# Kernel tuning notes

Measured on AMD Instinct MI355X. Metric: run time of the kernel, lower is better.

## Reference

```python
import jax, jax.numpy as jnp
import numpy as np
from jax import lax

BS, T, NN, F_IN = 4, 32, 128, 64
HID, HEADS, NC, LD, RH = 64, 4, 32, 64, 256
E = 2048
NEG_SLOPE = 0.2


def setup_inputs() -> dict:
    key = jax.random.key(0)
    ks = jax.random.split(key, 20)
    f32 = jnp.float32
    def n(k, shape, s=0.05):
        return jax.random.normal(k, shape, f32) * s
    G4 = 4 * RH
    return {
        "x": jax.random.normal(ks[0], (BS, T, NN, F_IN), f32),
        "edge_index": jax.random.randint(ks[1], (2, E), 0, NN),
        "W1": n(ks[2], (F_IN, HEADS * HID)),
        "as1": n(ks[3], (HEADS, HID)), "ad1": n(ks[4], (HEADS, HID)),
        "b1": jnp.zeros((HEADS * HID,), f32),
        "W2": n(ks[5], (HEADS * HID, HEADS * HID)),
        "as2": n(ks[6], (HEADS, HID)), "ad2": n(ks[7], (HEADS, HID)),
        "b2": jnp.zeros((HEADS * HID,), f32),
        "W3": n(ks[8], (HEADS * HID, HID)),
        "as3": n(ks[9], (1, HID)), "ad3": n(ks[10], (1, HID)),
        "b3": jnp.zeros((HID,), f32),
        "Wih_f": n(ks[11], (G4, HID)), "Whh_f": n(ks[12], (G4, RH)),
        "bih_f": jnp.zeros((G4,), f32), "bhh_f": jnp.zeros((G4,), f32),
        "Wih_b": n(ks[13], (G4, HID)), "Whh_b": n(ks[14], (G4, RH)),
        "bih_b": jnp.zeros((G4,), f32), "bhh_b": jnp.zeros((G4,), f32),
        "Wmu": n(ks[15], (NC * LD, 2 * RH)), "bmu": jnp.zeros((NC * LD,), f32),
        "Wlv": n(ks[16], (NC * LD, 2 * RH)), "blv": jnp.zeros((NC * LD,), f32),
        "Wpi": n(ks[17], (NC, 2 * RH)), "bpi": jnp.zeros((NC,), f32),
    }


def _lstm_dir(seq, Wih, Whh, bih, bhh, rh):
    # seq: [T, B, D]; torch gate order i, f, g, o
    B = seq.shape[1]
    h0 = jnp.zeros((B, rh), seq.dtype)
    c0 = jnp.zeros((B, rh), seq.dtype)
    def step(carry, xt):
        h, c = carry
        g = xt @ Wih.T + h @ Whh.T + bih + bhh
        i, f, gg, o = jnp.split(g, 4, axis=-1)
        c = jax.nn.sigmoid(f) * c + jax.nn.sigmoid(i) * jnp.tanh(gg)
        h = jax.nn.sigmoid(o) * jnp.tanh(c)
        return (h, c), None
    (hT, _), _ = lax.scan(step, (h0, c0), seq)
    return hT


def reference(x, edge_index, W1, as1, ad1, b1, W2, as2, ad2, b2,
              W3, as3, ad3, b3,
              Wih_f, Whh_f, bih_f, bhh_f, Wih_b, Whh_b, bih_b, bhh_b,
              Wmu, bmu, Wlv, blv, Wpi, bpi):
    bs, T_, nn_, fin = x.shape
    G = bs * T_
    N = G * nn_
    xt = x.reshape(N, fin)
    # batch the per-graph edge list with node offsets, then add self loops (PyG default)
    off = jnp.arange(G, dtype=edge_index.dtype) * nn_
    src = (edge_index[0][None, :] + off[:, None]).reshape(-1)
    dst = (edge_index[1][None, :] + off[:, None]).reshape(-1)
    loop = jnp.arange(N, dtype=edge_index.dtype)
    src = jnp.concatenate([src, loop])
    dst = jnp.concatenate([dst, loop])

    def gat(h_in, W, a_s, a_d, b, heads):
        C = W.shape[1] // heads
        h = (h_in @ W).reshape(N, heads, C)
        a_src = jnp.sum(h * a_s, axis=-1)  # [N, H]
        a_dst = jnp.sum(h * a_d, axis=-1)
        e = jax.nn.leaky_relu(a_src[src] + a_dst[dst], NEG_SLOPE)  # [Etot, H]
        m = jax.ops.segment_max(e, dst, num_segments=N)
        m = jnp.where(jnp.isfinite(m), m, 0.0)
        ex = jnp.exp(e - m[dst])
        den = jax.ops.segment_sum(ex, dst, num_segments=N)
        alpha = ex / (den[dst] + 1e-16)
        out = jax.ops.segment_sum(alpha[:, :, None] * h[src], dst, num_segments=N)
        return out.reshape(N, heads * C) + b

    h = jax.nn.relu(gat(xt, W1, as1, ad1, b1, HEADS))
    h = jax.nn.relu(gat(h, W2, as2, ad2, b2, HEADS))
    h = jax.nn.relu(gat(h, W3, as3, ad3, b3, 1))

    batch_idx = jnp.repeat(jnp.arange(G), nn_)
    graph_embs = jax.ops.segment_sum(h, batch_idx, num_segments=G).reshape(bs, T_, -1)
    seq = jnp.transpose(graph_embs, (1, 0, 2))  # [T, B, D]
    h_f = _lstm_dir(seq, Wih_f, Whh_f, bih_f, bhh_f, RH)
    h_b = _lstm_dir(seq[::-1], Wih_b, Whh_b, bih_b, bhh_b, RH)
    feat = jnp.concatenate([h_f, h_b], axis=-1)  # [B, 2*RH]
    mu = (feat @ Wmu.T + bmu).reshape(bs, NC, LD)
    logvar = (feat @ Wlv.T + blv).reshape(bs, NC, LD)
    pi_logits = feat @ Wpi.T + bpi
    return (mu, logvar, pi_logits)
```

## Files before the change

### kernel.cpp

```cpp
#include <hip/hip_runtime.h>
#include <hip/hip_bf16.h>
#include <cstdint>

#define NLOC 128
#define NGRAPH 128
#define NNODE 16384
#define EBASE 2048

typedef _Float16 half2v __attribute__((ext_vector_type(2)));
typedef _Float16 f16x8 __attribute__((ext_vector_type(8)));
typedef float f32x4 __attribute__((ext_vector_type(4)));

__device__ __forceinline__ float sigf(float x) { return 1.f / (1.f + __expf(-x)); }
__device__ __forceinline__ float tanhfast(float x) {
    float e = __expf(2.f * x);
    return 1.f - 2.f / (e + 1.f);
}
__device__ __forceinline__ uint32_t packh2(float a, float b) {
    half2v v;
    v.x = (_Float16)a; v.y = (_Float16)b;
    return __builtin_bit_cast(uint32_t, v);
}
__device__ __forceinline__ float dot2(uint32_t w, uint32_t h, float acc) {
#if __has_builtin(__builtin_amdgcn_fdot2)
    return __builtin_amdgcn_fdot2(__builtin_bit_cast(half2v, w),
                                  __builtin_bit_cast(half2v, h), acc, false);
#else
    half2v wv = __builtin_bit_cast(half2v, w);
    half2v hv = __builtin_bit_cast(half2v, h);
    return acc + (float)wv.x * (float)hv.x + (float)wv.y * (float)hv.y;
#endif
}

__global__ __launch_bounds__(256) void prep_kernel(const int* __restrict__ ei,
                                                   float* __restrict__ Adj,
                                                   const float* __restrict__ W1,
                                                   const float* __restrict__ W2,
                                                   const float* __restrict__ W3,
                                                   _Float16* __restrict__ W1t,
                                                   _Float16* __restrict__ W2t,
                                                   _Float16* __restrict__ W3t,
                                                   const float* __restrict__ Whh_f,
                                                   const float* __restrict__ Whh_b,
                                                   uint32_t* __restrict__ wreg,
                                                   uint32_t* __restrict__ wtail) {
    int b = blockIdx.x, tid = threadIdx.x;
    if (b < 128) {
        __shared__ int rowA[NLOC];
        int v = b;
        if (tid < NLOC) rowA[tid] = 0;
        __syncthreads();
        const int* srcs = ei;
        const int* dsts = ei + EBASE;
        int e0 = tid * 8;
#pragma unroll
        for (int k = 0; k < 8; ++k)
            if (dsts[e0 + k] == v) atomicAdd(&rowA[srcs[e0 + k]], 1);
        __syncthreads();
        if (tid < NLOC) Adj[v * NLOC + tid] = (float)rowA[tid] + (tid == v ? 1.f : 0.f);
    } else if (b < 144) {
        int i = (b - 128) * 1024 + tid * 4;
        int n = i >> 6, k = i & 63;
#pragma unroll
        for (int j = 0; j < 4; ++j) W1t[n * 64 + k + j] = (_Float16)W1[(size_t)(k + j) * 256 + n];
    } else if (b < 208) {
        int i = (b - 144) * 1024 + tid * 4;
        int n = i >> 8, k = i & 255;
#pragma unroll
        for (int j = 0; j < 4; ++j) W2t[n * 256 + k + j] = (_Float16)W2[(size_t)(k + j) * 256 + n];
    } else if (b < 224) {
        int i = (b - 208) * 1024 + tid * 4;
        int n = i >> 8, k = i & 255;
#pragma unroll
        for (int j = 0; j < 4; ++j) W3t[n * 256 + k + j] = (_Float16)W3[(size_t)(k + j) * 64 + n];
    } else {
        int gid = (b - 224) * 256 + tid;
        int dir = gid >> 10, row = gid & 1023;
        const float* src = (dir ? Whh_b : Whh_f) + (size_t)row * 256;
        uint4* wr4 = (uint4*)wreg;
#pragma unroll
        for (int i = 0; i < 24; ++i) {
            uint4 v;
            v.x = packh2(src[i * 8 + 0], src[i * 8 + 1]);
            v.y = packh2(src[i * 8 + 2], src[i * 8 + 3]);
            v.z = packh2(src[i * 8 + 4], src[i * 8 + 5]);
            v.w = packh2(src[i * 8 + 6], src[i * 8 + 7]);
            wr4[(size_t)(dir * 24 + i) * 1024 + row] = v;
        }
        uint4* wt4 = (uint4*)wtail;
#pragma unroll
        for (int ku = 0; ku < 8; ++ku) {
            const float* s8 = src + 192 + ku * 8;
            uint4 v;
            v.x = packh2(s8[0], s8[1]);
            v.y = packh2(s8[2], s8[3]);
            v.z = packh2(s8[4], s8[5]);
            v.w = packh2(s8[6], s8[7]);
            wt4[(size_t)(dir * 8 + ku) * 1024 + row] = v;
        }
    }
}

template <int K, int N, bool POOLX>
__global__ __launch_bounds__(512) void fl_kernel(const float* __restrict__ A,
                                                 const _Float16* __restrict__ Wg,
                                                 const float* __restrict__ a_s,
                                                 const float* __restrict__ a_d,
                                                 const float* __restrict__ Adj,
                                                 const float* __restrict__ bias,
                                                 const float* __restrict__ Wih_f, const float* __restrict__ bif, const float* __restrict__ bhf,
                                                 const float* __restrict__ Wih_b, const float* __restrict__ bib, const float* __restrict__ bhb,
                                                 float* __restrict__ outG) {
    constexpr int H = N / 64;
    constexpr int NT = N / 64;
    constexpr int LDA = K + 4;
    constexpr int LDB = 68;
    constexpr int LDH = 136;
    constexpr int ASB = 128 * LDA * 2;
    constexpr int HTB = N * LDH * 2;
    constexpr int R1 = (ASB > HTB) ? ASB : HTB;
    constexpr int R2 = 128 * LDH * 2;
    __shared__ __align__(16) char raw[R1 + R2];
    _Float16* As = (_Float16*)raw;
    _Float16* Ht = (_Float16*)raw;
    _Float16* Bs = (_Float16*)(raw + R1);
    _Float16* Wt = (_Float16*)(raw + R1);
    __shared__ float as_l[128 * H];
    __shared__ float ad_l[128 * H];
    __shared__ float den_l[128];
    __shared__ float as_part[4][128];
    __shared__ float ad_part[4][128];
    __shared__ float psum[8][64];
    __shared__ float emb[64];

    int g = blockIdx.x, tid = threadIdx.x;
    int lane = tid & 63, w = tid >> 6;
    int wm = w >> 2, wn = w & 3;
    int col = lane & 15, kg = lane >> 4;
    size_t base = (size_t)g * 128;

    float asc[NT], adc[NT];
#pragma unroll
    for (int nt = 0; nt < NT; ++nt) {
        int f = (wn * NT + nt) * 16 + col;
        asc[nt] = a_s[f];
        adc[nt] = a_d[f];
    }
    {
        const float* src = A + base * K;
        for (int i = tid; i < 128 * K / 2; i += 512) {
            int m = (2 * i) / K, k = (2 * i) % K;
            float2 v = *(const float2*)(src + (size_t)m * K + k);
            *(uint32_t*)&As[m * LDA + k] = packh2(v.x, v.y);
        }
    }
    f32x4 acc[4][NT];
#pragma unroll
    for (int mt = 0; mt < 4; ++mt)
#pragma unroll
        for (int nt = 0; nt < NT; ++nt) acc[mt][nt] = (f32x4){0.f, 0.f, 0.f, 0.f};
#pragma unroll 1
    for (int kc = 0; kc < K / 64; ++kc) {
        __syncthreads();
        for (int j = tid; j < N * 8; j += 512) {
            int n = j >> 3, ko = (j & 7) * 8;
            *(uint4*)&Bs[n * LDB + ko] = *(const uint4*)&Wg[(size_t)n * K + kc * 64 + ko];
        }
        __syncthreads();
        uint4 bf[NT][2];
#pragma unroll
        for (int nt = 0; nt < NT; ++nt) {
            int nb = (wn * NT + nt) * 16 + col;
            bf[nt][0] = *(const uint4*)&Bs[nb * LDB + kg * 8];
            bf[nt][1] = *(const uint4*)&Bs[nb * LDB + 32 + kg * 8];
        }
#pragma unroll
        for (int mt = 0; mt < 4; ++mt) {
            int mrow = wm * 64 + mt * 16 + col;
            uint4 a0 = *(const uint4*)&As[mrow * LDA + kc * 64 + kg * 8];
            uint4 a1 = *(const uint4*)&As[mrow * LDA + kc * 64 + 32 + kg * 8];
#pragma unroll
            for (int nt = 0; nt < NT; ++nt) {
                acc[mt][nt] = __builtin_amdgcn_mfma_f32_16x16x32_f16(
                    __builtin_bit_cast(f16x8, a0), __builtin_bit_cast(f16x8, bf[nt][0]),
                    acc[mt][nt], 0, 0, 0);
                acc[mt][nt] = __builtin_amdgcn_mfma_f32_16x16x32_f16(
                    __builtin_bit_cast(f16x8, a1), __builtin_bit_cast(f16x8, bf[nt][1]),
                    acc[mt][nt], 0, 0, 0);
            }
        }
    }
    __syncthreads();
#pragma unroll
    for (int mt = 0; mt < 4; ++mt) {
        int mb = wm * 64 + mt * 16;
        float pas[4] = {0.f, 0.f, 0.f, 0.f}, pdd[4] = {0.f, 0.f, 0.f, 0.f};
#pragma unroll
        for (int nt = 0; nt < NT; ++nt) {
#pragma unroll
            for (int r = 0; r < 4; ++r) {
                float hv = acc[mt][nt][r];
                pas[r] += hv * asc[nt];
                pdd[r] += hv * adc[nt];
            }
            int f = (wn * NT + nt) * 16 + col;
            *(uint32_t*)&Ht[f * LDH + mb + kg * 4] = packh2(acc[mt][nt][0], acc[mt][nt][1]);
            *(uint32_t*)&Ht[f * LDH + mb + kg * 4 + 2] = packh2(acc[mt][nt][2], acc[mt][nt][3]);
        }
#pragma unroll
        for (int off = 1; off < 16; off <<= 1)
#pragma unroll
            for (int r = 0; r < 4; ++r) {
                pas[r] += __shfl_xor(pas[r], off, 64);
                pdd[r] += __shfl_xor(pdd[r], off, 64);
            }
        if (col == 0) {
#pragma unroll
            for (int r = 0; r < 4; ++r) {
                int m = mb + kg * 4 + r;
                if constexpr (N == 256) {
                    as_l[m * 4 + wn] = pas[r];
                    ad_l[m * 4 + wn] = pdd[r];
                } else {
                    as_part[wn][m] = pas[r];
                    ad_part[wn][m] = pdd[r];
                }
            }
        }
    }
    __syncthreads();
    if constexpr (N == 64) {
        if (tid < 128) {
            as_l[tid] = as_part[0][tid] + as_part[1][tid] + as_part[2][tid] + as_part[3][tid];
            ad_l[tid] = ad_part[0][tid] + ad_part[1][tid] + ad_part[2][tid] + ad_part[3][tid];
        }
        __syncthreads();
    }
    for (int h = 0; h < H; ++h) {
        {
            int v = tid >> 2, ub = (tid & 3) * 32;
            float advv = ad_l[v * H + h];
            const float* arow = Adj + (size_t)v * 128 + ub;
            float dsum = 0.f;
#pragma unroll
            for (int j = 0; j < 16; ++j) {
                float a0 = arow[2 * j], a1 = arow[2 * j + 1];
                float e0 = as_l[(ub + 2 * j) * H + h] + advv;
                float e1 = as_l[(ub + 2 * j + 1) * H + h] + advv;
                e0 = (e0 > 0.f) ? e0 : 0.2f * e0;
                e1 = (e1 > 0.f) ? e1 : 0.2f * e1;
                float w0 = a0 * __expf(e0);
                float w1 = a1 * __expf(e1);
                dsum += w0 + w1;
                *(uint32_t*)&Wt[v * LDH + ub + 2 * j] = packh2(w0, w1);
            }
            dsum += __shfl_xor(dsum, 1, 64);
            dsum += __shfl_xor(dsum, 2, 64);
            if ((tid & 3) == 0) den_l[v] = dsum;
        }
        __syncthreads();
        {
            int vt = w;
            f16x8 af[4];
#pragma unroll
            for (int kt = 0; kt < 4; ++kt) {
                uint4 au = *(const uint4*)&Wt[(vt * 16 + col) * LDH + kt * 32 + kg * 8];
                af[kt] = __builtin_bit_cast(f16x8, au);
            }
            float dn[4];
#pragma unroll
            for (int r = 0; r < 4; ++r) dn[r] = den_l[vt * 16 + kg * 4 + r] + 1e-16f;
#pragma unroll
            for (int ft = 0; ft < 4; ++ft) {
                int f = h * 64 + ft * 16 + col;
                f32x4 oacc = {0.f, 0.f, 0.f, 0.f};
#pragma unroll
                for (int kt = 0; kt < 4; ++kt) {
                    uint4 bu = *(const uint4*)&Ht[f * LDH + kt * 32 + kg * 8];
                    oacc = __builtin_amdgcn_mfma_f32_16x16x32_f16(
                        af[kt], __builtin_bit_cast(f16x8, bu), oacc, 0, 0, 0);
                }
                float bv = bias[f];
                if constexpr (!POOLX) {
#pragma unroll
                    for (int r = 0; r < 4; ++r) {
                        int v = vt * 16 + kg * 4 + r;
                        float o = oacc[r] / dn[r] + bv;
                        outG[(size_t)(base + v) * N + f] = fmaxf(o, 0.f);
                    }
                } else {
                    float ps = 0.f;
#pragma unroll
                    for (int r = 0; r < 4; ++r) ps += fmaxf(oacc[r] / dn[r] + bv, 0.f);
                    ps += __shfl_xor(ps, 16, 64);
                    ps += __shfl_xor(ps, 32, 64);
                    if (kg == 0) psum[w][f] = ps;
                }
            }
        }
        __syncthreads();
    }
    if constexpr (POOLX) {
        if (tid < 64) {
            float s = 0.f;
#pragma unroll
            for (int q = 0; q < 8; ++q) s += psum[q][tid];
            emb[tid] = s;
        }
        __syncthreads();
        int rrow = (g & 31) * 4 + (g >> 5);
        for (int dir = 0; dir < 2; ++dir) {
            const float* W = dir ? Wih_b : Wih_f;
            const float* bi = dir ? bib : bif;
            const float* bh = dir ? bhb : bhf;
            for (int o = tid; o < 1024; o += 512) {
                const float* wr = W + (size_t)o * 64;
                float s = bi[o] + bh[o];
#pragma unroll
                for (int k = 0; k < 64; k += 4) {
                    float4 wv = *(const float4*)(wr + k);
                    s += emb[k] * wv.x + emb[k + 1] * wv.y + emb[k + 2] * wv.z + emb[k + 3] * wv.w;
                }
                outG[dir * 131072 + rrow * 1024 + o] = s;
            }
        }
    }
}

__global__ __launch_bounds__(1024, 1) void lstm_kernel(const float* __restrict__ xp,
                                                       const uint32_t* __restrict__ wreg,
                                                       const uint32_t* __restrict__ wtail,
                                                       float* __restrict__ hT) {
    int blk = blockIdx.x;
    int dir = blk >> 2, batch = blk & 3;
    int t = threadIdx.x;
    uint32_t wa[96];
    {
        const uint4* ra = (const uint4*)wreg + (size_t)dir * 24 * 1024;
#pragma unroll
        for (int i = 0; i < 24; ++i) {
            uint4 v = ra[i * 1024 + t];
            wa[i * 4 + 0] = v.x; wa[i * 4 + 1] = v.y; wa[i * 4 + 2] = v.z; wa[i * 4 + 3] = v.w;
        }
    }
    __shared__ __align__(16) uint4 wlds[8 * 1024];
    __shared__ __align__(16) uint32_t h_pk[128];
    __shared__ float gv[1024];
    {
        const uint4* tsrc = (const uint4*)wtail + (size_t)dir * 8 * 1024;
        for (int i = t; i < 8 * 1024; i += 1024) wlds[i] = tsrc[i];
    }
    if (t < 128) h_pk[t] = 0;
    __syncthreads();
    float creg = 0.f;
    const float* xpb = xp + dir * 131072 + batch * 1024;
#pragma unroll 1
    for (int step = 0; step < 32; ++step) {
        int teff = dir ? (31 - step) : step;
        float xa = xpb[teff * 4096 + t];
        float acc = 0.f;
#pragma unroll
        for (int q = 0; q < 24; ++q) {
            uint4 hq = *(const uint4*)&h_pk[q * 4];
            acc = dot2(wa[q * 4 + 0], hq.x, acc);
            acc = dot2(wa[q * 4 + 1], hq.y, acc);
            acc = dot2(wa[q * 4 + 2], hq.z, acc);
            acc = dot2(wa[q * 4 + 3], hq.w, acc);
        }
#pragma unroll
        for (int ku = 0; ku < 8; ++ku) {
            uint4 hq = *(const uint4*)&h_pk[96 + ku * 4];
            uint4 qa = wlds[ku * 1024 + t];
            acc = dot2(qa.x, hq.x, acc); acc = dot2(qa.y, hq.y, acc);
            acc = dot2(qa.z, hq.z, acc); acc = dot2(qa.w, hq.w, acc);
        }
        gv[t] = acc + xa;
        __syncthreads();
        if (t < 256) {
            float iv = gv[t], fv = gv[t + 256], gg = gv[t + 512], ov = gv[t + 768];
            creg = sigf(fv) * creg + sigf(iv) * tanhfast(gg);
            float hv = sigf(ov) * tanhfast(creg);
            if (step == 31) hT[(size_t)(dir * 4 + batch) * 256 + t] = hv;
            float hnext = __shfl_down(hv, 1, 64);
            if ((t & 1) == 0) h_pk[t >> 1] = packh2(hv, hnext);
        }
        __syncthreads();
    }
}

__global__ __launch_bounds__(256) void heads_kernel(const float* __restrict__ hT,
                                                    const float* __restrict__ Wmu, const float* __restrict__ bmu,
                                                    const float* __restrict__ Wlv, const float* __restrict__ blv,
                                                    const float* __restrict__ Wpi, const float* __restrict__ bpi,
                                                    float* __restrict__ out) {
    __shared__ __align__(16) float feat[4][512];
    int tid = threadIdx.x;
    for (int i = tid; i < 2048; i += 256) {
        int b = i >> 9, j = i & 511;
        int d = j >> 8, jj = j & 255;
        feat[b][j] = hT[(size_t)(d * 4 + b) * 256 + jj];
    }
    __syncthreads();
    int o = blockIdx.x * 32 + (tid >> 3);
    int kp = tid & 7;
    if (o >= 4128) return;
    const float* Wr;
    float bv;
    int kind, m;
    if (o < 2048) { Wr = Wmu + (size_t)o * 512; bv = bmu[o]; kind = 0; m = o; }
    else if (o < 4096) { m = o - 2048; Wr = Wlv + (size_t)m * 512; bv = blv[m]; kind = 1; }
    else { m = o - 4096; Wr = Wpi + (size_t)m * 512; bv = bpi[m]; kind = 2; }
    float s0 = 0.f, s1 = 0.f, s2 = 0.f, s3 = 0.f;
    int k0 = kp * 64;
#pragma unroll
    for (int j = 0; j < 16; ++j) {
        int k = k0 + j * 4;
        float4 wv = *(const float4*)(Wr + k);
        s0 += feat[0][k] * wv.x + feat[0][k + 1] * wv.y + feat[0][k + 2] * wv.z + feat[0][k + 3] * wv.w;
        s1 += feat[1][k] * wv.x + feat[1][k + 1] * wv.y + feat[1][k + 2] * wv.z + feat[1][k + 3] * wv.w;
        s2 += feat[2][k] * wv.x + feat[2][k + 1] * wv.y + feat[2][k + 2] * wv.z + feat[2][k + 3] * wv.w;
        s3 += feat[3][k] * wv.x + feat[3][k + 1] * wv.y + feat[3][k + 2] * wv.z + feat[3][k + 3] * wv.w;
    }
#pragma unroll
    for (int off = 1; off < 8; off <<= 1) {
        s0 += __shfl_xor(s0, off, 64);
        s1 += __shfl_xor(s1, off, 64);
        s2 += __shfl_xor(s2, off, 64);
        s3 += __shfl_xor(s3, off, 64);
    }
    if (kp != 0) return;
    s0 += bv; s1 += bv; s2 += bv; s3 += bv;
    if (kind == 0) {
        out[0 * 2048 + m] = s0; out[1 * 2048 + m] = s1; out[2 * 2048 + m] = s2; out[3 * 2048 + m] = s3;
    } else if (kind == 1) {
        out[8192 + 0 * 2048 + m] = s0; out[8192 + 1 * 2048 + m] = s1;
        out[8192 + 2 * 2048 + m] = s2; out[8192 + 3 * 2048 + m] = s3;
    } else {
        out[16384 + 0 * 32 + m] = s0; out[16384 + 1 * 32 + m] = s1;
        out[16384 + 2 * 32 + m] = s2; out[16384 + 3 * 32 + m] = s3;
    }
}

extern "C" void kernel_launch(void* const* d_in, const int* in_sizes, int n_in,
                              void* d_out, int out_size, void* d_ws, size_t ws_size,
                              hipStream_t stream) {
    const float* x = (const float*)d_in[0];
    const int* ei = (const int*)d_in[1];
    const float* W1 = (const float*)d_in[2];
    const float* as1 = (const float*)d_in[3];
    const float* ad1 = (const float*)d_in[4];
    const float* b1 = (const float*)d_in[5];
    const float* W2 = (const float*)d_in[6];
    const float* as2 = (const float*)d_in[7];
    const float* ad2 = (const float*)d_in[8];
    const float* b2 = (const float*)d_in[9];
    const float* W3 = (const float*)d_in[10];
    const float* as3 = (const float*)d_in[11];
    const float* ad3 = (const float*)d_in[12];
    const float* b3 = (const float*)d_in[13];
    const float* Wih_f = (const float*)d_in[14];
    const float* Whh_f = (const float*)d_in[15];
    const float* bih_f = (const float*)d_in[16];
    const float* bhh_f = (const float*)d_in[17];
    const float* Wih_b = (const float*)d_in[18];
    const float* Whh_b = (const float*)d_in[19];
    const float* bih_b = (const float*)d_in[20];
    const float* bhh_b = (const float*)d_in[21];
    const float* Wmu = (const float*)d_in[22];
    const float* bmu = (const float*)d_in[23];
    const float* Wlv = (const float*)d_in[24];
    const float* blv = (const float*)d_in[25];
    const float* Wpi = (const float*)d_in[26];
    const float* bpi = (const float*)d_in[27];

    float* ws = (float*)d_ws;
    float* buf1 = ws;
    float* buf2 = ws + 4194304;
    float* Adj = ws + 8388608;
    float* xp = ws + 8404992;
    float* hT = ws + 8667136;
    _Float16* W1t = (_Float16*)(ws + 8669184);
    _Float16* W2t = (_Float16*)(ws + 8677376);
    _Float16* W3t = (_Float16*)(ws + 8710144);
    uint32_t* wreg = (uint32_t*)(ws + 8718336);
    uint32_t* wtail = wreg + 196608;
    float* out = (float*)d_out;

    prep_kernel<<<232, 256, 0, stream>>>(ei, Adj, W1, W2, W3, W1t, W2t, W3t,
                                         Whh_f, Whh_b, wreg, wtail);
    fl_kernel<64, 256, false><<<128, 512, 0, stream>>>(x, W1t, as1, ad1, Adj, b1,
        Wih_f, bih_f, bhh_f, Wih_b, bih_b, bhh_b, buf1);
    fl_kernel<256, 256, false><<<128, 512, 0, stream>>>(buf1, W2t, as2, ad2, Adj, b2,
        Wih_f, bih_f, bhh_f, Wih_b, bih_b, bhh_b, buf2);
    fl_kernel<256, 64, true><<<128, 512, 0, stream>>>(buf2, W3t, as3, ad3, Adj, b3,
        Wih_f, bih_f, bhh_f, Wih_b, bih_b, bhh_b, xp);
    lstm_kernel<<<8, 1024, 0, stream>>>(xp, wreg, wtail, hT);
    heads_kernel<<<129, 256, 0, stream>>>(hT, Wmu, bmu, Wlv, blv, Wpi, bpi, out);
}
```

Measured before the change: 211.9 us.

## Split GAT layer kernels across feature halves to double block count

The first two GAT layers now launch a 2D grid where each block handles 128 of the 256 output features (two heads) for one graph, instead of all 256. This doubles the number of workgroups from 128 to 256 so the GPU's compute units are better filled. Per-head attention-logit partial sums are now always gathered through the per-wave partial arrays and reduced per local head. In exchange, each block re-stages the full input activation tile, so input loads and the fp16 conversion are duplicated across the two halves.

```diff
diff --git a/kernel.cpp b/kernel.cpp
--- a/kernel.cpp
+++ b/kernel.cpp
@@ -101,7 +101,7 @@
     }
 }
 
-template <int K, int N, bool POOLX>
+template <int K, int NL, int NF, bool POOLX>
 __global__ __launch_bounds__(512) void fl_kernel(const float* __restrict__ A,
                                                  const _Float16* __restrict__ Wg,
                                                  const float* __restrict__ a_s,
@@ -111,13 +111,14 @@
                                                  const float* __restrict__ Wih_f, const float* __restrict__ bif, const float* __restrict__ bhf,
                                                  const float* __restrict__ Wih_b, const float* __restrict__ bib, const float* __restrict__ bhb,
                                                  float* __restrict__ outG) {
-    constexpr int H = N / 64;
-    constexpr int NT = N / 64;
+    constexpr int HL = NL / 64;
+    constexpr int NT = NL / 64;
+    constexpr int WPH = 4 / HL;
     constexpr int LDA = K + 4;
     constexpr int LDB = 68;
     constexpr int LDH = 136;
     constexpr int ASB = 128 * LDA * 2;
-    constexpr int HTB = N * LDH * 2;
+    constexpr int HTB = NL * LDH * 2;
     constexpr int R1 = (ASB > HTB) ? ASB : HTB;
     constexpr int R2 = 128 * LDH * 2;
     __shared__ __align__(16) char raw[R1 + R2];
@@ -125,8 +126,8 @@
     _Float16* Ht = (_Float16*)raw;
     _Float16* Bs = (_Float16*)(raw + R1);
     _Float16* Wt = (_Float16*)(raw + R1);
-    __shared__ float as_l[128 * H];
-    __shared__ float ad_l[128 * H];
+    __shared__ float as_l[128 * HL];
+    __shared__ float ad_l[128 * HL];
     __shared__ float den_l[128];
     __shared__ float as_part[4][128];
     __shared__ float ad_part[4][128];
@@ -134,6 +135,7 @@
     __shared__ float emb[64];
 
     int g = blockIdx.x, tid = threadIdx.x;
+    int foff = blockIdx.y * NL;
     int lane = tid & 63, w = tid >> 6;
     int wm = w >> 2, wn = w & 3;
     int col = lane & 15, kg = lane >> 4;
@@ -142,7 +144,7 @@
     float asc[NT], adc[NT];
 #pragma unroll
     for (int nt = 0; nt < NT; ++nt) {
-        int f = (wn * NT + nt) * 16 + col;
+        int f = foff + (wn * NT + nt) * 16 + col;
         asc[nt] = a_s[f];
         adc[nt] = a_d[f];
     }
@@ -162,9 +164,9 @@
 #pragma unroll 1
     for (int kc = 0; kc < K / 64; ++kc) {
         __syncthreads();
-        for (int j = tid; j < N * 8; j += 512) {
+        for (int j = tid; j < NL * 8; j += 512) {
             int n = j >> 3, ko = (j & 7) * 8;
-            *(uint4*)&Bs[n * LDB + ko] = *(const uint4*)&Wg[(size_t)n * K + kc * 64 + ko];
+            *(uint4*)&Bs[n * LDB + ko] = *(const uint4*)&Wg[(size_t)(foff + n) * K + kc * 64 + ko];
         }
         __syncthreads();
         uint4 bf[NT][2];
@@ -218,35 +220,37 @@
 #pragma unroll
             for (int r = 0; r < 4; ++r) {
                 int m = mb + kg * 4 + r;
-                if constexpr (N == 256) {
-                    as_l[m * 4 + wn] = pas[r];
-                    ad_l[m * 4 + wn] = pdd[r];
-                } else {
-                    as_part[wn][m] = pas[r];
-                    ad_part[wn][m] = pdd[r];
-                }
+                as_part[wn][m] = pas[r];
+                ad_part[wn][m] = pdd[r];
             }
         }
     }
     __syncthreads();
-    if constexpr (N == 64) {
-        if (tid < 128) {
-            as_l[tid] = as_part[0][tid] + as_part[1][tid] + as_part[2][tid] + as_part[3][tid];
-            ad_l[tid] = ad_part[0][tid] + ad_part[1][tid] + ad_part[2][tid] + ad_part[3][tid];
-        }
-        __syncthreads();
-    }
-    for (int h = 0; h < H; ++h) {
+    if (tid < 128) {
+#pragma unroll
+        for (int hl = 0; hl < HL; ++hl) {
+            float sa = 0.f, sd = 0.f;
+#pragma unroll
+            for (int q = 0; q < WPH; ++q) {
+                sa += as_part[hl * WPH + q][tid];
+                sd += ad_part[hl * WPH + q][tid];
+            }
+            as_l[tid * HL + hl] = sa;
+            ad_l[tid * HL + hl] = sd;
+        }
+    }
+    __syncthreads();
+    for (int h = 0; h < HL; ++h) {
         {
             int v = tid >> 2, ub = (tid & 3) * 32;
-            float advv = ad_l[v * H + h];
+            float advv = ad_l[v * HL + h];
             const float* arow = Adj + (size_t)v * 128 + ub;
             float dsum = 0.f;
 #pragma unroll
             for (int j = 0; j < 16; ++j) {
                 float a0 = arow[2 * j], a1 = arow[2 * j + 1];
-                float e0 = as_l[(ub + 2 * j) * H + h] + advv;
-                float e1 = as_l[(ub + 2 * j + 1) * H + h] + advv;
+                float e0 = as_l[(ub + 2 * j) * HL + h] + advv;
+                float e1 = as_l[(ub + 2 * j + 1) * HL + h] + advv;
                 e0 = (e0 > 0.f) ? e0 : 0.2f * e0;
                 e1 = (e1 > 0.f) ? e1 : 0.2f * e1;
                 float w0 = a0 * __expf(e0);
@@ -280,13 +284,13 @@
                     oacc = __builtin_amdgcn_mfma_f32_16x16x32_f16(
                         af[kt], __builtin_bit_cast(f16x8, bu), oacc, 0, 0, 0);
                 }
-                float bv = bias[f];
+                float bv = bias[foff + f];
                 if constexpr (!POOLX) {
 #pragma unroll
                     for (int r = 0; r < 4; ++r) {
                         int v = vt * 16 + kg * 4 + r;
                         float o = oacc[r] / dn[r] + bv;
-                        outG[(size_t)(base + v) * N + f] = fmaxf(o, 0.f);
+                        outG[(size_t)(base + v) * NF + foff + f] = fmaxf(o, 0.f);
                     }
                 } else {
                     float ps = 0.f;
@@ -488,11 +492,11 @@
 
     prep_kernel<<<232, 256, 0, stream>>>(ei, Adj, W1, W2, W3, W1t, W2t, W3t,
                                          Whh_f, Whh_b, wreg, wtail);
-    fl_kernel<64, 256, false><<<128, 512, 0, stream>>>(x, W1t, as1, ad1, Adj, b1,
+    fl_kernel<64, 128, 256, false><<<dim3(128, 2), 512, 0, stream>>>(x, W1t, as1, ad1, Adj, b1,
         Wih_f, bih_f, bhh_f, Wih_b, bih_b, bhh_b, buf1);
-    fl_kernel<256, 256, false><<<128, 512, 0, stream>>>(buf1, W2t, as2, ad2, Adj, b2,
+    fl_kernel<256, 128, 256, false><<<dim3(128, 2), 512, 0, stream>>>(buf1, W2t, as2, ad2, Adj, b2,
         Wih_f, bih_f, bhh_f, Wih_b, bih_b, bhh_b, buf2);
-    fl_kernel<256, 64, true><<<128, 512, 0, stream>>>(buf2, W3t, as3, ad3, Adj, b3,
+    fl_kernel<256, 64, 64, true><<<dim3(128, 1), 512, 0, stream>>>(buf2, W3t, as3, ad3, Adj, b3,
         Wih_f, bih_f, bhh_f, Wih_b, bih_b, bhh_b, xp);
     lstm_kernel<<<8, 1024, 0, stream>>>(xp, wreg, wtail, hT);
     heads_kernel<<<129, 256, 0, stream>>>(hT, Wmu, bmu, Wlv, blv, Wpi, bpi, out);
```

Result: faster. 193.6 us (median of 2 runs) (-8.6%).
